# Performance work log

Hardware: AMD Instinct MI355X
Metric: run time of the kernel (lower is better)

The kernel has to match this reference:

```python
import jax, jax.numpy as jnp
import numpy as np

ALPHA = 0.2  # LeakyReLU negative slope
EDGE_NUM = 3


def _gat(q_nodes, v, adj, a_q, a_v):
    # q_nodes: (b,n,d_hidden), v: (b,n,d_model), adj: (b,n,n)
    # e_ij = LeakyReLU(a_q . h_i + a_v . v_j)  (decomposition of a^T[h_i;v_j])
    s_q = jnp.einsum('bnd,d->bn', q_nodes, a_q)
    s_v = jnp.einsum('bne,e->bn', v, a_v)
    e = jax.nn.leaky_relu(s_q[:, :, None] + s_v[:, None, :], negative_slope=ALPHA)
    e = jnp.where(adj > 0, e, -1e9)
    attn = jax.nn.softmax(e, axis=-1)           # (b,n,n)
    return jnp.einsum('bij,bje->bie', attn, v)  # (b,n,d_model)


def setup_inputs() -> dict:
    key = jax.random.key(0)
    ks = jax.random.split(key, 16)
    b, n, dh, dm = 8, 1024, 512, 512
    s = 0.02
    inp = {
        'nodes': jax.random.normal(ks[0], (b, n, dh), dtype=jnp.float32),
        'mask': jax.random.randint(ks[1], (2, b, n, n), 0, 2, dtype=jnp.int32),
        'node_type': jax.random.randint(ks[2], (b, n), 0, 5, dtype=jnp.int64),
        # edge-typed linears (bias=False), stacked over 3 edge types
        'W_in': jax.random.normal(ks[3], (EDGE_NUM, dh, dm), dtype=jnp.float32) * s,
        'W_out': jax.random.normal(ks[4], (EDGE_NUM, dh, dm), dtype=jnp.float32) * s,
        # GAT attention vectors, split into query / value halves
        'a_in_q': jax.random.normal(ks[5], (dh,), dtype=jnp.float32) * s,
        'a_in_v': jax.random.normal(ks[6], (dm,), dtype=jnp.float32) * s,
        'a_out_q': jax.random.normal(ks[7], (dh,), dtype=jnp.float32) * s,
        'a_out_v': jax.random.normal(ks[8], (dm,), dtype=jnp.float32) * s,
        # GGNN propagator (reset / update / transform)
        'W_r': jax.random.normal(ks[9], (3 * dm, dm), dtype=jnp.float32) * s,
        'b_r': jnp.zeros((dm,), dtype=jnp.float32),
        'W_z': jax.random.normal(ks[10], (3 * dm, dm), dtype=jnp.float32) * s,
        'b_z': jnp.zeros((dm,), dtype=jnp.float32),
        'W_t': jax.random.normal(ks[11], (3 * dm, dm), dtype=jnp.float32) * s,
        'b_t': jnp.zeros((dm,), dtype=jnp.float32),
    }
    return inp


def reference(nodes, mask, node_type, W_in, W_out, a_in_q, a_in_v, a_out_q, a_out_v,
              W_r, b_r, W_z, b_z, W_t, b_t):
    # type masks for tags 2,3,4 -> (3,b,n)
    tags = jnp.arange(2, 2 + EDGE_NUM, dtype=node_type.dtype)
    tmask = (node_type[None, :, :] == tags[:, None, None]).astype(nodes.dtype)
    # edge-typed linear + masked sum over edge types
    node_in = jnp.sum(jnp.einsum('bnd,tde->tbne', nodes, W_in) * tmask[..., None], axis=0)
    node_out = jnp.sum(jnp.einsum('bnd,tde->tbne', nodes, W_out) * tmask[..., None], axis=0)
    # GAT-style masked attention (in / out edges); dropout = identity (eval)
    h_in = _gat(nodes, node_in, mask[0], a_in_q, a_in_v)
    h_out = _gat(nodes, node_out, mask[1], a_out_q, a_out_v)
    # GGNN gated propagator
    a = jnp.concatenate([h_in, h_out, nodes], axis=-1)
    r = jax.nn.sigmoid(a @ W_r + b_r)
    z = jax.nn.sigmoid(a @ W_z + b_z)
    joint = jnp.concatenate([h_in, h_out, r * nodes], axis=-1)
    h_hat = jnp.tanh(joint @ W_t + b_t)
    return (1.0 - z) * nodes + z * h_hat
```

## Files before the change

kernel.cpp:

```cpp
#include <hip/hip_runtime.h>
#include <hip/hip_bf16.h>
#include <stdint.h>

typedef unsigned short u16;
typedef __attribute__((ext_vector_type(8))) short bf16x8;
typedef __attribute__((ext_vector_type(4))) float floatx4;

__device__ __forceinline__ float bf2f(u16 v){ return __uint_as_float(((unsigned)v)<<16); }
__device__ __forceinline__ u16 f2bf(float f){
  unsigned u = __float_as_uint(f);
  unsigned r = 0x7fffu + ((u>>16)&1u);
  return (u16)((u+r)>>16);
}
__device__ __forceinline__ float lrelu(float x){ return x > 0.f ? x : 0.2f*x; }
__device__ __forceinline__ float sigm(float t){
  t = fminf(fmaxf(t, -30.f), 30.f);
  return 1.f/(1.f + __expf(-t));
}

#define GLOAD16(ldsdst, gsrc) \
  __builtin_amdgcn_global_load_lds((const __attribute__((address_space(1))) void*)(gsrc), \
      (__attribute__((address_space(3))) void*)(ldsdst), 16, 0, 0)

__global__ void k_detect(const u16* __restrict__ nodes_raw,
                         const int* __restrict__ ntype_raw, int* flags)
{
  __shared__ int s_wild, s_nz;
  if (threadIdx.x == 0){ s_wild = 0; s_nz = 0; }
  __syncthreads();
  int wild = 0;
#pragma unroll
  for (int i = 0; i < 16; i++){
    u16 w = nodes_raw[threadIdx.x*16 + i];
    int e = (w >> 7) & 0xFF;
    if (e != 0 && (e < 102 || e > 152)) wild++;
  }
  int nz = 0;
  if (threadIdx.x < 255 && ntype_raw[2*threadIdx.x + 1] != 0) nz = 1;
  atomicAdd(&s_wild, wild);
  atomicAdd(&s_nz, nz);
  __syncthreads();
  if (threadIdx.x == 0){
    flags[0] = (s_wild > 1024) ? 1 : 0;
    flags[1] = (s_nz == 0) ? 1 : 0;
  }
}

struct CanonDesc {
  const void* src[13];
  u16*        dst[13];
  int startBlk[13];
  int n4[13];
};
__global__ __launch_bounds__(256)
void k_canon_all(CanonDesc d, u16* __restrict__ X, const int* __restrict__ flags)
{
  int blk = blockIdx.x;
  int seg = 0;
#pragma unroll
  for (int s = 1; s < 13; s++) if (blk >= d.startBlk[s]) seg = s;
  int i = (blk - d.startBlk[seg])*256 + threadIdx.x;
  if (i >= d.n4[seg]) return;
  uint2 bits;
  if (flags[0]) {
    float4 v = ((const float4*)d.src[seg])[i];
    ushort4 o2;
    o2.x = f2bf(v.x); o2.y = f2bf(v.y); o2.z = f2bf(v.z); o2.w = f2bf(v.w);
    bits = *(uint2*)&o2;
  } else {
    bits = ((const uint2*)d.src[seg])[i];
  }
  ((uint2*)d.dst[seg])[i] = bits;
  if (seg == 0) {
    int e0 = i*4;
    long r = e0 >> 9;
    int  c = e0 & 511;
    *(uint2*)&X[r*2048 + c] = bits;
  }
}

__global__ void k_build_idx(const int* __restrict__ ntype, const int* __restrict__ flags,
                            int* __restrict__ idx, int* __restrict__ cnt)
{
  __shared__ int c[3];
  if (threadIdx.x < 3) c[threadIdx.x] = 0;
  __syncthreads();
  const int i64 = flags[1];
  for (int i = threadIdx.x; i < 8192; i += 256){
    int t = i64 ? ntype[2*i] : ntype[i];
    if (t >= 2 && t <= 4){
      int p = atomicAdd(&c[t-2], 1);
      idx[(t-2)*8192 + p] = i;
    }
  }
  __syncthreads();
  if (threadIdx.x < 3) cnt[threadIdx.x] = c[threadIdx.x];
}

template<int MODE, class Epi>
__global__ __launch_bounds__(256)
void gemm_bt(const u16* __restrict__ A, int ldA, long sAz,
             const u16* __restrict__ B, int ldB, long sBz,
             int K, Epi epi)
{
  __shared__ __align__(16) u16 As[4][128][32];
  __shared__ __align__(16) u16 Bs[4][128][32];
  int bm, bn, bz;
  if (MODE == 0){ bm = blockIdx.x; bn = blockIdx.y; bz = blockIdx.z; }
  else          { bz = blockIdx.x; bn = blockIdx.y; bm = blockIdx.z; }
  const int tid  = threadIdx.x;
  const int lane = tid & 63;
  const int wave = tid >> 6;
  const int wm = (wave & 1) << 6;
  const int wn = (wave >> 1) << 6;
  const int mrow = lane & 15;
  const int quad = lane >> 4;

  const u16* Ab = A + (long)bz*sAz + (long)bm*128*ldA;
  const u16* Bb = B + (long)bz*sBz + (long)bn*128*ldB;
  const int srow = tid >> 2;
  const int scol = (tid & 3) << 3;
  const u16* gA0 = Ab + (long)srow*ldA + scol;
  const u16* gA1 = Ab + (long)(srow+64)*ldA + scol;
  const u16* gB0 = Bb + (long)srow*ldB + scol;
  const u16* gB1 = Bb + (long)(srow+64)*ldB + scol;

  floatx4 acc[4][4];
#pragma unroll
  for (int i=0;i<4;i++)
#pragma unroll
    for (int j=0;j<4;j++) acc[i][j] = 0.f;

  auto issue = [&](int buf){
    GLOAD16(&As[buf][srow][scol],    gA0);
    GLOAD16(&As[buf][srow+64][scol], gA1);
    GLOAD16(&Bs[buf][srow][scol],    gB0);
    GLOAD16(&Bs[buf][srow+64][scol], gB1);
    gA0 += 32; gA1 += 32; gB0 += 32; gB1 += 32;
  };

  issue(0); issue(1); issue(2);
  const int nIter = K >> 5;
  for (int it = 0; it < nIter; ++it) {
    const int cur = it & 3;
    const int rem = nIter - 1 - it;
    if (rem >= 2)      asm volatile("s_waitcnt vmcnt(8)" ::: "memory");
    else if (rem == 1) asm volatile("s_waitcnt vmcnt(4)" ::: "memory");
    else               asm volatile("s_waitcnt vmcnt(0)" ::: "memory");
    asm volatile("s_barrier" ::: "memory");
    if (it + 3 < nIter) issue((it + 3) & 3);
    bf16x8 af[4], bfr[4];
#pragma unroll
    for (int i=0;i<4;i++) af[i]  = *(const bf16x8*)&As[cur][wm + i*16 + mrow][quad*8];
#pragma unroll
    for (int i=0;i<4;i++) bfr[i] = *(const bf16x8*)&Bs[cur][wn + i*16 + mrow][quad*8];
#pragma unroll
    for (int mi=0;mi<4;mi++)
#pragma unroll
      for (int ni=0;ni<4;ni++)
        acc[mi][ni] = __builtin_amdgcn_mfma_f32_16x16x32_bf16(af[mi], bfr[ni], acc[mi][ni], 0,0,0);
  }

#pragma unroll
  for (int mi=0;mi<4;mi++)
#pragma unroll
    for (int ni=0;ni<4;ni++) {
      const int col  = (bn<<7) + wn + ni*16 + mrow;
      const int row0 = (bm<<7) + wm + mi*16 + quad*4;
#pragma unroll
      for (int r=0;r<4;r++)
        epi(row0 + r, col, bz, acc[mi][ni][r]);
    }
}

__global__ __launch_bounds__(256)
void gemm_typed(const u16* __restrict__ A, const u16* __restrict__ B,
                const int* __restrict__ idx, const int* __restrict__ cnt,
                u16* __restrict__ node_in, u16* __restrict__ node_out)
{
  const int bz = blockIdx.z;
  const int count = cnt[bz];
  const int m0 = blockIdx.x << 7;
  if (m0 >= count) return;
  __shared__ __align__(16) u16 As[4][128][32];
  __shared__ __align__(16) u16 Bs[4][128][32];
  const int bn = blockIdx.y;
  const int tid  = threadIdx.x;
  const int lane = tid & 63;
  const int wave = tid >> 6;
  const int wm = (wave & 1) << 6;
  const int wn = (wave >> 1) << 6;
  const int mrow = lane & 15;
  const int quad = lane >> 4;
  const int* myidx = idx + bz*8192;

  const int srow = tid >> 2;
  const int scol = (tid & 3) << 3;
  int r0i = m0 + srow;      if (r0i >= count) r0i = m0;
  int r1i = m0 + srow + 64; if (r1i >= count) r1i = m0;
  const u16* gA0 = A + (long)myidx[r0i]*512 + scol;
  const u16* gA1 = A + (long)myidx[r1i]*512 + scol;
  const u16* Bb = B + (long)bz*1024*512 + (long)bn*128*512;
  const u16* gB0 = Bb + (long)srow*512 + scol;
  const u16* gB1 = Bb + (long)(srow+64)*512 + scol;

  floatx4 acc[4][4];
#pragma unroll
  for (int i=0;i<4;i++)
#pragma unroll
    for (int j=0;j<4;j++) acc[i][j] = 0.f;

  auto issue = [&](int buf){
    GLOAD16(&As[buf][srow][scol],    gA0);
    GLOAD16(&As[buf][srow+64][scol], gA1);
    GLOAD16(&Bs[buf][srow][scol],    gB0);
    GLOAD16(&Bs[buf][srow+64][scol], gB1);
    gA0 += 32; gA1 += 32; gB0 += 32; gB1 += 32;
  };

  issue(0); issue(1); issue(2);
  for (int it = 0; it < 16; ++it) {
    const int cur = it & 3;
    const int rem = 15 - it;
    if (rem >= 2)      asm volatile("s_waitcnt vmcnt(8)" ::: "memory");
    else if (rem == 1) asm volatile("s_waitcnt vmcnt(4)" ::: "memory");
    else               asm volatile("s_waitcnt vmcnt(0)" ::: "memory");
    asm volatile("s_barrier" ::: "memory");
    if (it + 3 < 16) issue((it + 3) & 3);
    bf16x8 af[4], bfr[4];
#pragma unroll
    for (int i=0;i<4;i++) af[i]  = *(const bf16x8*)&As[cur][wm + i*16 + mrow][quad*8];
#pragma unroll
    for (int i=0;i<4;i++) bfr[i] = *(const bf16x8*)&Bs[cur][wn + i*16 + mrow][quad*8];
#pragma unroll
    for (int mi=0;mi<4;mi++)
#pragma unroll
      for (int ni=0;ni<4;ni++)
        acc[mi][ni] = __builtin_amdgcn_mfma_f32_16x16x32_bf16(af[mi], bfr[ni], acc[mi][ni], 0,0,0);
  }

#pragma unroll
  for (int mi=0;mi<4;mi++) {
    const int lr0 = wm + mi*16 + quad*4;
#pragma unroll
    for (int r=0;r<4;r++) {
      const int lr = lr0 + r;
      if (m0 + lr >= count) continue;
      const long orig = myidx[m0 + lr];
#pragma unroll
      for (int ni=0;ni<4;ni++) {
        const int col = (bn<<7) + wn + ni*16 + mrow;
        u16 h = f2bf(acc[mi][ni][r]);
        if (col < 512) node_in [orig*512 + col]       = h;
        else           node_out[orig*512 + (col-512)] = h;
      }
    }
  }
}

struct EpiPV {
  const float* il; u16* X;
  __device__ void operator()(int row, int col, int bz, float v) const {
    long gr = (long)(bz & 7)*1024 + row;
    int colOff = 512 + ((bz >> 3) << 9);
    X[gr*2048 + colOff + col] = f2bf(v * il[(long)(bz>>3)*8192 + gr]);
  }
};
struct EpiG1 {
  const u16* nodes; const u16* b_r; const u16* b_z; u16* X; u16* zbuf;
  __device__ void operator()(int row, int col, int bz, float v) const {
    if (col < 512) {
      float r = sigm(v + bf2f(b_r[col]));
      X[(long)row*2048 + 1536 + col] = f2bf(r * bf2f(nodes[(long)row*512 + col]));
    } else {
      int c = col - 512;
      zbuf[(long)row*512 + c] = f2bf(sigm(v + bf2f(b_z[c])));
    }
  }
};
struct EpiG2 {
  const u16* zbuf; const u16* nodes; const u16* b_t; const int* flags; void* out;
  __device__ void operator()(int row, int col, int bz, float v) const {
    long idx = (long)row*512 + col;
    float t = fminf(fmaxf(v + bf2f(b_t[col]), -15.f), 15.f);
    float h = 2.f*sigm(2.f*t) - 1.f;
    float z = bf2f(zbuf[idx]);
    float nv = bf2f(nodes[idx]);
    float o2 = (1.f - z)*nv + z*h;
    if (flags[0]) ((float*)out)[idx] = o2;
    else          ((u16*)out)[idx]   = f2bf(o2);
  }
};

struct TrDesc {
  const u16* src[9]; u16* dst[9]; int rot[9]; int ldD[9]; int rows[9]; int modK[9];
};
__global__ __launch_bounds__(256)
void k_wtrans(TrDesc d)
{
  __shared__ u16 tile[32][33];
  const int z = blockIdx.z;
  const int r0 = blockIdx.y*32;
  if (r0 >= d.rows[z]) return;
  const u16* src = d.src[z];
  u16* dst = d.dst[z];
  const int c0 = blockIdx.x*32;
  const int tx = threadIdx.x, ty = threadIdx.y;
#pragma unroll
  for (int i=0;i<32;i+=8)
    tile[ty+i][tx] = src[(long)(r0+ty+i)*512 + c0 + tx];
  __syncthreads();
  const int k0 = (r0 + d.rot[z]) % d.modK[z];
#pragma unroll
  for (int i=0;i<32;i+=8)
    dst[(long)(c0+ty+i)*d.ldD[z] + k0 + tx] = tile[tx][ty+i];
}

__global__ __launch_bounds__(256)
void k_vtrans(const u16* __restrict__ nin, const u16* __restrict__ nout,
              u16* __restrict__ vin, u16* __restrict__ vout)
{
  __shared__ u16 tile[32][33];
  const int z = blockIdx.z;
  const int b = z & 7;
  const u16* src = (z < 8 ? nin : nout) + (long)b*1024*512;
  u16* dst = (z < 8 ? vin : vout) + (long)b*512*1024;
  const int c0 = blockIdx.x*32, r0 = blockIdx.y*32;
  const int tx = threadIdx.x, ty = threadIdx.y;
#pragma unroll
  for (int i=0;i<32;i+=8)
    tile[ty+i][tx] = src[(long)(r0+ty+i)*512 + c0 + tx];
  __syncthreads();
#pragma unroll
  for (int i=0;i<32;i+=8)
    dst[(long)(c0+ty+i)*1024 + r0 + tx] = tile[tx][ty+i];
}

__device__ __forceinline__ void load8f(float* f, const u16* p){
  uint4 q = *(const uint4*)p;
  unsigned w[4] = {q.x, q.y, q.z, q.w};
#pragma unroll
  for (int i=0;i<4;i++){ f[2*i] = bf2f((u16)(w[i]&0xffffu)); f[2*i+1] = bf2f((u16)(w[i]>>16)); }
}

__global__ __launch_bounds__(256)
void k_svec(const u16* __restrict__ nodes, const u16* __restrict__ nin, const u16* __restrict__ nout,
            const u16* __restrict__ aiq, const u16* __restrict__ aiv,
            const u16* __restrict__ aoq, const u16* __restrict__ aov,
            float* sq_all, float* sv_all)
{
  const int lane = threadIdx.x & 63, wave = threadIdx.x >> 6;
  const long row = (long)blockIdx.x*4 + wave;
  const int c = lane << 3;
  float xn[8], xi[8], xo[8], q1[8], v1[8], q2[8], v2[8];
  load8f(xn, nodes + row*512 + c);
  load8f(xi, nin   + row*512 + c);
  load8f(xo, nout  + row*512 + c);
  load8f(q1, aiq + c); load8f(v1, aiv + c);
  load8f(q2, aoq + c); load8f(v2, aov + c);
  float s0=0,s1=0,s2=0,s3=0;
#pragma unroll
  for (int j=0;j<8;j++){ s0 += xn[j]*q1[j]; s1 += xn[j]*q2[j]; s2 += xi[j]*v1[j]; s3 += xo[j]*v2[j]; }
#pragma unroll
  for (int off=32; off; off>>=1){
    s0 += __shfl_xor(s0, off);
    s1 += __shfl_xor(s1, off);
    s2 += __shfl_xor(s2, off);
    s3 += __shfl_xor(s3, off);
  }
  if (lane==0){
    sq_all[row] = s0; sq_all[8192 + row] = s1;
    sv_all[row] = s2; sv_all[8192 + row] = s3;
  }
}

__global__ __launch_bounds__(256)
void k_stats(const int* __restrict__ mask, const float* __restrict__ sq_all,
             const float* __restrict__ sv_all, u16* __restrict__ P, float* __restrict__ il_all)
{
  const int lane = threadIdx.x & 63, wave = threadIdx.x >> 6;
  const long row = (long)blockIdx.x*4 + wave;
  const long gr  = (long)blockIdx.y*8192 + row;
  const int* mrow = mask + gr*1024;
  const float* svb = sv_all + (long)blockIdx.y*8192 + (row >> 10)*1024;
  const float qs = sq_all[gr];
  float m = -3.0e38f;
  float e[4][4];
#pragma unroll
  for (int it=0; it<4; ++it) {
    int j = it*256 + lane*4;
    int4 mk = *(const int4*)&mrow[j];
    float4 s = *(const float4*)&svb[j];
    e[it][0] = mk.x > 0 ? lrelu(qs + s.x) : -1e9f;
    e[it][1] = mk.y > 0 ? lrelu(qs + s.y) : -1e9f;
    e[it][2] = mk.z > 0 ? lrelu(qs + s.z) : -1e9f;
    e[it][3] = mk.w > 0 ? lrelu(qs + s.w) : -1e9f;
    m = fmaxf(m, fmaxf(fmaxf(e[it][0], e[it][1]), fmaxf(e[it][2], e[it][3])));
  }
#pragma unroll
  for (int off=32; off; off>>=1) m = fmaxf(m, __shfl_xor(m, off));
  float l = 0.f;
#pragma unroll
  for (int it=0; it<4; ++it) {
    int j = it*256 + lane*4;
    float p0 = __expf(e[it][0] - m), p1 = __expf(e[it][1] - m);
    float p2 = __expf(e[it][2] - m), p3 = __expf(e[it][3] - m);
    ushort4 pk;
    pk.x = f2bf(p0); pk.y = f2bf(p1); pk.z = f2bf(p2); pk.w = f2bf(p3);
    *(ushort4*)&P[gr*1024 + j] = pk;
    l += (p0 + p1) + (p2 + p3);
  }
#pragma unroll
  for (int off=32; off; off>>=1) l += __shfl_xor(l, off);
  if (lane==0) il_all[gr] = 1.f / l;
}

extern "C" void kernel_launch(void* const* d_in, const int* in_sizes, int n_in,
                              void* d_out, int out_size, void* d_ws, size_t ws_size,
                              hipStream_t stream)
{
  const void* nodes_r = d_in[0];
  const int*  mask    = (const int*)d_in[1];
  const int*  ntype   = (const int*)d_in[2];

  char* base = (char*)d_ws;
  size_t o = 0;
  auto alloc = [&](size_t bytes){ void* p = base + o; o += (bytes + 255) & ~size_t(255); return p; };
  int*  flags   = (int*)alloc(256);
  int*  cnt     = (int*)alloc(256);
  int*  idx     = (int*)alloc(3ll*8192*4);
  u16* cn_nodes = (u16*)alloc(8192ll*512*2);
  u16* cn_Win   = (u16*)alloc(3ll*512*512*2);
  u16* cn_Wout  = (u16*)alloc(3ll*512*512*2);
  u16* cn_Wr    = (u16*)alloc(1536ll*512*2);
  u16* cn_Wz    = (u16*)alloc(1536ll*512*2);
  u16* cn_Wt    = (u16*)alloc(1536ll*512*2);
  u16* cn_aiq   = (u16*)alloc(512*2);
  u16* cn_aiv   = (u16*)alloc(512*2);
  u16* cn_aoq   = (u16*)alloc(512*2);
  u16* cn_aov   = (u16*)alloc(512*2);
  u16* cn_br    = (u16*)alloc(512*2);
  u16* cn_bz    = (u16*)alloc(512*2);
  u16* cn_bt    = (u16*)alloc(512*2);
  u16* node_in  = (u16*)alloc(8192ll*512*2);
  u16* node_out = (u16*)alloc(8192ll*512*2);
  u16* Vt       = (u16*)alloc(16ll*512*1024*2);
  u16* X        = (u16*)alloc(8192ll*2048*2);
  u16* P        = (u16*)alloc(16ll*1024*1024*2);
  u16* Wio_t    = (u16*)alloc(3ll*1024*512*2);
  u16* Wrz_t    = (u16*)alloc(1024ll*1536*2);
  u16* Wt_t     = (u16*)alloc(512ll*1536*2);
  float* sq_all = (float*)alloc(16384*4);
  float* sv_all = (float*)alloc(16384*4);
  float* il_all = (float*)alloc(16384*4);
  u16* zbuf = node_in;

  hipMemsetAsync(node_in, 0, 2ll*8192*512*2, stream);

  k_detect<<<1, 256, 0, stream>>>((const u16*)nodes_r, ntype, flags);

  CanonDesc cd;
  const int canonN[13] = {8192*512, 3*512*512, 3*512*512, 1536*512, 1536*512, 1536*512,
                          512,512,512,512,512,512,512};
  u16* canonDst[13] = {cn_nodes, cn_Win, cn_Wout, cn_Wr, cn_Wz, cn_Wt,
                       cn_aiq, cn_aiv, cn_aoq, cn_aov, cn_br, cn_bz, cn_bt};
  const int canonSrcIdx[13] = {0,3,4,9,11,13,5,6,7,8,10,12,14};
  int blk = 0;
  for (int s=0;s<13;s++){
    cd.src[s] = d_in[canonSrcIdx[s]];
    cd.dst[s] = canonDst[s];
    cd.n4[s]  = canonN[s]/4;
    cd.startBlk[s] = blk;
    blk += (cd.n4[s] + 255)/256;
  }
  k_canon_all<<<blk, 256, 0, stream>>>(cd, X, flags);

  k_build_idx<<<1, 256, 0, stream>>>(ntype, flags, idx, cnt);

  TrDesc td;
  td.src[0]=cn_Wr; td.src[1]=cn_Wz; td.src[2]=cn_Wt;
  td.dst[0]=Wrz_t; td.dst[1]=Wrz_t + 512ll*1536; td.dst[2]=Wt_t;
  td.rot[0]=512; td.rot[1]=512; td.rot[2]=0;
  td.ldD[0]=1536; td.ldD[1]=1536; td.ldD[2]=1536;
  td.rows[0]=1536; td.rows[1]=1536; td.rows[2]=1536;
  td.modK[0]=1536; td.modK[1]=1536; td.modK[2]=1536;
  for (int t=0;t<3;t++){
    td.src[3+t]=cn_Win  + (long)t*512*512; td.dst[3+t]=Wio_t + (long)t*1024*512;
    td.src[6+t]=cn_Wout + (long)t*512*512; td.dst[6+t]=Wio_t + (long)t*1024*512 + 512ll*512;
    td.rot[3+t]=td.rot[6+t]=0; td.ldD[3+t]=td.ldD[6+t]=512;
    td.rows[3+t]=td.rows[6+t]=512; td.modK[3+t]=td.modK[6+t]=512;
  }
  k_wtrans<<<dim3(16,48,9), dim3(32,8), 0, stream>>>(td);

  gemm_typed<<<dim3(64,8,3), 256, 0, stream>>>(cn_nodes, Wio_t, idx, cnt, node_in, node_out);

  k_vtrans<<<dim3(16,32,16), dim3(32,8), 0, stream>>>(node_in, node_out, Vt, Vt + 8ll*512*1024);

  k_svec<<<2048, 256, 0, stream>>>(cn_nodes, node_in, node_out, cn_aiq, cn_aiv, cn_aoq, cn_aov,
                                   sq_all, sv_all);

  k_stats<<<dim3(2048,2), 256, 0, stream>>>(mask, sq_all, sv_all, P, il_all);

  gemm_bt<1><<<dim3(16,4,8), 256, 0, stream>>>(P, 1024, 1024ll*1024, Vt, 1024, 512ll*1024, 1024,
                                               EpiPV{il_all, X});

  gemm_bt<0><<<dim3(64,8,1), 256, 0, stream>>>(X, 2048, 0ll, Wrz_t, 1536, 0ll, 1536,
                                               EpiG1{cn_nodes, cn_br, cn_bz, X, zbuf});
  gemm_bt<0><<<dim3(64,4,1), 256, 0, stream>>>(X + 512, 2048, 0ll, Wt_t, 1536, 0ll, 1536,
                                               EpiG2{zbuf, cn_nodes, cn_bt, flags, (void*)d_out});
}
```

Baseline: 375.0 us.

## Replace LDS-staged GEMM pipeline with direct global-to-register double buffering

Both GEMM kernels stop staging A and B tiles through shared memory with async global-to-LDS loads, barriers and waitcnt. Each lane now loads its MFMA fragments straight from global memory into registers, alternating between two register buffers so the next k-slice loads while the current one is multiplied. This removes LDS traffic and block-wide barriers. In exchange, each operand row is fetched by both waves that share it instead of once per block, so more global or L2 traffic is issued, and the extra fragment registers may lower occupancy.

```diff
diff --git a/kernel.cpp b/kernel.cpp
--- a/kernel.cpp
+++ b/kernel.cpp
@@ -17,10 +17,6 @@
   t = fminf(fmaxf(t, -30.f), 30.f);
   return 1.f/(1.f + __expf(-t));
 }
-
-#define GLOAD16(ldsdst, gsrc) \
-  __builtin_amdgcn_global_load_lds((const __attribute__((address_space(1))) void*)(gsrc), \
-      (__attribute__((address_space(3))) void*)(ldsdst), 16, 0, 0)
 
 __global__ void k_detect(const u16* __restrict__ nodes_raw,
                          const int* __restrict__ ntype_raw, int* flags)
@@ -103,8 +99,6 @@
              const u16* __restrict__ B, int ldB, long sBz,
              int K, Epi epi)
 {
-  __shared__ __align__(16) u16 As[4][128][32];
-  __shared__ __align__(16) u16 Bs[4][128][32];
   int bm, bn, bz;
   if (MODE == 0){ bm = blockIdx.x; bn = blockIdx.y; bz = blockIdx.z; }
   else          { bz = blockIdx.x; bn = blockIdx.y; bm = blockIdx.z; }
@@ -116,14 +110,13 @@
   const int mrow = lane & 15;
   const int quad = lane >> 4;
 
-  const u16* Ab = A + (long)bz*sAz + (long)bm*128*ldA;
-  const u16* Bb = B + (long)bz*sBz + (long)bn*128*ldB;
-  const int srow = tid >> 2;
-  const int scol = (tid & 3) << 3;
-  const u16* gA0 = Ab + (long)srow*ldA + scol;
-  const u16* gA1 = Ab + (long)(srow+64)*ldA + scol;
-  const u16* gB0 = Bb + (long)srow*ldB + scol;
-  const u16* gB1 = Bb + (long)(srow+64)*ldB + scol;
+  const u16* pa[4];
+  const u16* pb[4];
+#pragma unroll
+  for (int i=0;i<4;i++){
+    pa[i] = A + bz*sAz + (long)(bm*128 + wm + i*16 + mrow)*ldA + quad*8;
+    pb[i] = B + bz*sBz + (long)(bn*128 + wn + i*16 + mrow)*ldB + quad*8;
+  }
 
   floatx4 acc[4][4];
 #pragma unroll
@@ -131,34 +124,41 @@
 #pragma unroll
     for (int j=0;j<4;j++) acc[i][j] = 0.f;
 
-  auto issue = [&](int buf){
-    GLOAD16(&As[buf][srow][scol],    gA0);
-    GLOAD16(&As[buf][srow+64][scol], gA1);
-    GLOAD16(&Bs[buf][srow][scol],    gB0);
-    GLOAD16(&Bs[buf][srow+64][scol], gB1);
-    gA0 += 32; gA1 += 32; gB0 += 32; gB1 += 32;
-  };
-
-  issue(0); issue(1); issue(2);
+  bf16x8 a0[4], b0[4], a1[4], b1[4];
+  auto ld0 = [&](int k0){
+#pragma unroll
+    for (int i=0;i<4;i++) a0[i] = *(const bf16x8*)(pa[i] + k0);
+#pragma unroll
+    for (int i=0;i<4;i++) b0[i] = *(const bf16x8*)(pb[i] + k0);
+  };
+  auto ld1 = [&](int k0){
+#pragma unroll
+    for (int i=0;i<4;i++) a1[i] = *(const bf16x8*)(pa[i] + k0);
+#pragma unroll
+    for (int i=0;i<4;i++) b1[i] = *(const bf16x8*)(pb[i] + k0);
+  };
+  auto fma0 = [&](){
+#pragma unroll
+    for (int mi=0;mi<4;mi++)
+#pragma unroll
+      for (int ni=0;ni<4;ni++)
+        acc[mi][ni] = __builtin_amdgcn_mfma_f32_16x16x32_bf16(a0[mi], b0[ni], acc[mi][ni], 0,0,0);
+  };
+  auto fma1 = [&](){
+#pragma unroll
+    for (int mi=0;mi<4;mi++)
+#pragma unroll
+      for (int ni=0;ni<4;ni++)
+        acc[mi][ni] = __builtin_amdgcn_mfma_f32_16x16x32_bf16(a1[mi], b1[ni], acc[mi][ni], 0,0,0);
+  };
+
   const int nIter = K >> 5;
-  for (int it = 0; it < nIter; ++it) {
-    const int cur = it & 3;
-    const int rem = nIter - 1 - it;
-    if (rem >= 2)      asm volatile("s_waitcnt vmcnt(8)" ::: "memory");
-    else if (rem == 1) asm volatile("s_waitcnt vmcnt(4)" ::: "memory");
-    else               asm volatile("s_waitcnt vmcnt(0)" ::: "memory");
-    asm volatile("s_barrier" ::: "memory");
-    if (it + 3 < nIter) issue((it + 3) & 3);
-    bf16x8 af[4], bfr[4];
-#pragma unroll
-    for (int i=0;i<4;i++) af[i]  = *(const bf16x8*)&As[cur][wm + i*16 + mrow][quad*8];
-#pragma unroll
-    for (int i=0;i<4;i++) bfr[i] = *(const bf16x8*)&Bs[cur][wn + i*16 + mrow][quad*8];
-#pragma unroll
-    for (int mi=0;mi<4;mi++)
-#pragma unroll
-      for (int ni=0;ni<4;ni++)
-        acc[mi][ni] = __builtin_amdgcn_mfma_f32_16x16x32_bf16(af[mi], bfr[ni], acc[mi][ni], 0,0,0);
+  ld0(0);
+  for (int it = 0; it < nIter; it += 2){
+    ld1((it+1) << 5);
+    fma0();
+    if (it + 2 < nIter) ld0((it+2) << 5);
+    fma1();
   }
 
 #pragma unroll
@@ -182,8 +182,6 @@
   const int count = cnt[bz];
   const int m0 = blockIdx.x << 7;
   if (m0 >= count) return;
-  __shared__ __align__(16) u16 As[4][128][32];
-  __shared__ __align__(16) u16 Bs[4][128][32];
   const int bn = blockIdx.y;
   const int tid  = threadIdx.x;
   const int lane = tid & 63;
@@ -194,15 +192,15 @@
   const int quad = lane >> 4;
   const int* myidx = idx + bz*8192;
 
-  const int srow = tid >> 2;
-  const int scol = (tid & 3) << 3;
-  int r0i = m0 + srow;      if (r0i >= count) r0i = m0;
-  int r1i = m0 + srow + 64; if (r1i >= count) r1i = m0;
-  const u16* gA0 = A + (long)myidx[r0i]*512 + scol;
-  const u16* gA1 = A + (long)myidx[r1i]*512 + scol;
-  const u16* Bb = B + (long)bz*1024*512 + (long)bn*128*512;
-  const u16* gB0 = Bb + (long)srow*512 + scol;
-  const u16* gB1 = Bb + (long)(srow+64)*512 + scol;
+  const u16* pa[4];
+  const u16* pb[4];
+#pragma unroll
+  for (int i=0;i<4;i++){
+    int r = m0 + wm + i*16 + mrow;
+    if (r >= count) r = count - 1;
+    pa[i] = A + (long)myidx[r]*512 + quad*8;
+    pb[i] = B + (long)bz*1024*512 + (long)(bn*128 + wn + i*16 + mrow)*512 + quad*8;
+  }
 
   floatx4 acc[4][4];
 #pragma unroll
@@ -210,33 +208,40 @@
 #pragma unroll
     for (int j=0;j<4;j++) acc[i][j] = 0.f;
 
-  auto issue = [&](int buf){
-    GLOAD16(&As[buf][srow][scol],    gA0);
-    GLOAD16(&As[buf][srow+64][scol], gA1);
-    GLOAD16(&Bs[buf][srow][scol],    gB0);
-    GLOAD16(&Bs[buf][srow+64][scol], gB1);
-    gA0 += 32; gA1 += 32; gB0 += 32; gB1 += 32;
-  };
-
-  issue(0); issue(1); issue(2);
-  for (int it = 0; it < 16; ++it) {
-    const int cur = it & 3;
-    const int rem = 15 - it;
-    if (rem >= 2)      asm volatile("s_waitcnt vmcnt(8)" ::: "memory");
-    else if (rem == 1) asm volatile("s_waitcnt vmcnt(4)" ::: "memory");
-    else               asm volatile("s_waitcnt vmcnt(0)" ::: "memory");
-    asm volatile("s_barrier" ::: "memory");
-    if (it + 3 < 16) issue((it + 3) & 3);
-    bf16x8 af[4], bfr[4];
-#pragma unroll
-    for (int i=0;i<4;i++) af[i]  = *(const bf16x8*)&As[cur][wm + i*16 + mrow][quad*8];
-#pragma unroll
-    for (int i=0;i<4;i++) bfr[i] = *(const bf16x8*)&Bs[cur][wn + i*16 + mrow][quad*8];
+  bf16x8 a0[4], b0[4], a1[4], b1[4];
+  auto ld0 = [&](int k0){
+#pragma unroll
+    for (int i=0;i<4;i++) a0[i] = *(const bf16x8*)(pa[i] + k0);
+#pragma unroll
+    for (int i=0;i<4;i++) b0[i] = *(const bf16x8*)(pb[i] + k0);
+  };
+  auto ld1 = [&](int k0){
+#pragma unroll
+    for (int i=0;i<4;i++) a1[i] = *(const bf16x8*)(pa[i] + k0);
+#pragma unroll
+    for (int i=0;i<4;i++) b1[i] = *(const bf16x8*)(pb[i] + k0);
+  };
+  auto fma0 = [&](){
 #pragma unroll
     for (int mi=0;mi<4;mi++)
 #pragma unroll
       for (int ni=0;ni<4;ni++)
-        acc[mi][ni] = __builtin_amdgcn_mfma_f32_16x16x32_bf16(af[mi], bfr[ni], acc[mi][ni], 0,0,0);
+        acc[mi][ni] = __builtin_amdgcn_mfma_f32_16x16x32_bf16(a0[mi], b0[ni], acc[mi][ni], 0,0,0);
+  };
+  auto fma1 = [&](){
+#pragma unroll
+    for (int mi=0;mi<4;mi++)
+#pragma unroll
+      for (int ni=0;ni<4;ni++)
+        acc[mi][ni] = __builtin_amdgcn_mfma_f32_16x16x32_bf16(a1[mi], b1[ni], acc[mi][ni], 0,0,0);
+  };
+
+  ld0(0);
+  for (int it = 0; it < 16; it += 2){
+    ld1((it+1) << 5);
+    fma0();
+    if (it + 2 < 16) ld0((it+2) << 5);
+    fma1();
   }
 
 #pragma unroll
```

After: 502.0 us. +33.8%, slower.
